# Kernel tuning notes

Measured on AMD Instinct MI355X. Metric: run time of the kernel, lower is better.

Reference implementation:

```python
import jax, jax.numpy as jnp
import numpy as np

B, H, W, C = 4, 64, 64, 256


def _conv1x1(t, w, b):
    # 1x1 Conv2D == per-pixel matmul over channels (NHWC)
    return jnp.einsum('bhwc,cd->bhwd', t, w) + b


def setup_inputs() -> dict:
    key = jax.random.key(0)
    ks = jax.random.split(key, 12)
    s = 0.02
    inp = {
        'x': jax.random.normal(ks[0], (B, H, W, C), dtype=jnp.float32),
        'g': jax.random.normal(ks[1], (B, H, W, C), dtype=jnp.float32),
        'Wx1': jax.random.normal(ks[2], (C, C), dtype=jnp.float32) * s,
        'bx1': jnp.zeros((C,), dtype=jnp.float32),
        'Wx2': jax.random.normal(ks[3], (C, C), dtype=jnp.float32) * s,
        'bx2': jnp.zeros((C,), dtype=jnp.float32),
        'Wx3': jax.random.normal(ks[4], (C, C), dtype=jnp.float32) * s,
        'bx3': jnp.zeros((C,), dtype=jnp.float32),
        'Wg1': jax.random.normal(ks[5], (C, C), dtype=jnp.float32) * s,
        'bg1': jnp.zeros((C,), dtype=jnp.float32),
        'Wg2': jax.random.normal(ks[6], (C, C), dtype=jnp.float32) * s,
        'bg2': jnp.zeros((C,), dtype=jnp.float32),
    }
    return inp


def reference(x, g, Wx1, bx1, Wx2, bx2, Wx3, bx3, Wg1, bg1, Wg2, bg2):
    b, h, w, c = x.shape
    hw = h * w
    # x-branch projections, flattened to (B, HW, C)
    xw1 = _conv1x1(x, Wx1, bx1).reshape(b, hw, c)
    xw2 = _conv1x1(x, Wx2, bx2).reshape(b, hw, c)
    xw3 = _conv1x1(x, Wx3, bx3).reshape(b, hw, c)
    # g-branch projections
    gw1 = _conv1x1(g, Wg1, bg1).reshape(b, hw, c)
    gw2 = _conv1x1(g, Wg2, bg2).reshape(b, hw, c)
    # Dot(axes=(2,1))([xw_2, xw_1^T]) -> (B, HW, HW), softmax over last axis
    x_attn = jax.nn.softmax(jnp.einsum('bic,bjc->bij', xw2, xw1), axis=-1)
    g_attn = jax.nn.softmax(jnp.einsum('bic,bjc->bij', gw2, gw1), axis=-1)
    # elementwise gate then renormalize
    attn = jax.nn.softmax(x_attn * g_attn, axis=-1)
    # Keras Dot(axes=1): contract axis 1 of attn with axis 1 of xw3
    # out[b, j, c] = sum_i attn[b, i, j] * xw3[b, i, c]
    out = jnp.einsum('bij,bic->bjc', attn, xw3).reshape(b, h, w, c)
    return x + out
```

## Files before the change

kernel.cpp:

```cpp
#include <hip/hip_runtime.h>

typedef float f32x4 __attribute__((ext_vector_type(4)));
typedef short s16x8 __attribute__((ext_vector_type(8)));
typedef unsigned int u32x4 __attribute__((ext_vector_type(4)));
typedef unsigned char u8;
typedef unsigned short u16;
typedef unsigned int u32;
typedef unsigned long long u64;

#define NPOS 4096
#define CCH  256
#define MTOT 16384
#define PBYTES ((size_t)NPOS * NPOS * 2)

#define SZ_F8   ((size_t)MTOT * 256)
#define O_F8    ((size_t)0)
#define O_WT    (O_F8   + 4 * SZ_F8)
#define O_XW3T  (O_WT   + (size_t)5*256*256*2)
#define O_ZX    (O_XW3T + (size_t)MTOT*256*2)
#define O_ZG    (O_ZX   + (size_t)8*MTOT*4)
#define O_ID    (O_ZG   + (size_t)8*MTOT*4)
#define O_Z2    (O_ID   + (size_t)MTOT*4)
#define O_IZ2   (O_Z2   + (size_t)64*MTOT*4)
#define O_P     (O_IZ2  + (size_t)MTOT*4)

__device__ __forceinline__ u16 f2bf(float f) {
    u32 u = __builtin_bit_cast(u32, f);
    u32 r = (u + 0x7FFFu + ((u >> 16) & 1u)) >> 16;
    return (u16)r;
}
__device__ __forceinline__ float bf2f(u16 h) {
    u32 u = ((u32)h) << 16;
    return __builtin_bit_cast(float, u);
}
__device__ __forceinline__ u32 pk2(float a, float b) {
    return (u32)f2bf(a) | ((u32)f2bf(b) << 16);
}
__device__ __forceinline__ f32x4 mfma_bf16(s16x8 a, s16x8 b, f32x4 c) {
    return __builtin_amdgcn_mfma_f32_16x16x32_bf16(a, b, c, 0, 0, 0);
}
__device__ __forceinline__ f32x4 mfma_fp8(long a, long b, f32x4 c) {
    return __builtin_amdgcn_mfma_f32_16x16x32_fp8_fp8(a, b, c, 0, 0, 0);
}
__device__ __forceinline__ int xcd_swz(int bid, int nwg) {
    return (bid & 7) * (nwg >> 3) + (bid >> 3);
}
__device__ __forceinline__ u32x4 ntld(const void* p) {
    return __builtin_nontemporal_load((const u32x4*)p);
}
__device__ __forceinline__ void ntst(void* p, u32x4 v) {
    __builtin_nontemporal_store(v, (u32x4*)p);
}

__global__ __launch_bounds__(256) void prep_w(
    const float* __restrict__ W0, const float* __restrict__ W1,
    const float* __restrict__ W2, const float* __restrict__ W3,
    const float* __restrict__ W4, u32* __restrict__ wT)
{
    const int p = blockIdx.x, kq = blockIdx.y, n = threadIdx.x;
    const float* W = (p==0)?W0:(p==1)?W1:(p==2)?W2:(p==3)?W3:W4;
#pragma unroll 4
    for (int kk = 0; kk < 32; ++kk) {
        int k = kq*64 + kk*2;
        float v0 = W[k*256 + n];
        float v1 = W[(k+1)*256 + n];
        wT[(p*65536 + n*256 + k) >> 1] = pk2(v0, v1);
    }
}

__global__ __launch_bounds__(256) void proj_kernel(
    const float* __restrict__ x, const float* __restrict__ g,
    const float* __restrict__ bb0, const float* __restrict__ bb1,
    const float* __restrict__ bb2, const float* __restrict__ bb3,
    const float* __restrict__ bb4,
    const u16* __restrict__ wT, u8* __restrict__ f8, u8* __restrict__ xw3T)
{
    const int branch = blockIdx.y;
    const int m0 = blockIdx.x * 128;
    const float* A = branch ? g : x;
    __shared__ u8 sA[128*512];
    __shared__ u8 sC[128*512];
    const int t = threadIdx.x;
    const int l = t & 63, lr = l & 15, lg = l >> 4;
    const int wv = t >> 6, wm = wv >> 1, wn = wv & 1;

    {
        const int m = t >> 1, h = t & 1;
        const float* src = &A[(size_t)(m0 + m) * 256 + h * 128];
        const u32 dbase = m * 512;
#pragma unroll
        for (int c = 0; c < 16; ++c) {
            float4 a = *(const float4*)(src + c*8);
            float4 b = *(const float4*)(src + c*8 + 4);
            u32 pk[4] = { pk2(a.x, a.y), pk2(a.z, a.w), pk2(b.x, b.y), pk2(b.z, b.w) };
            int kbyte = h*256 + c*16;
            *(uint4*)&sA[dbase + (kbyte ^ ((m & 7) << 4))] = *(uint4*)pk;
        }
    }
    __syncthreads();

    const int np = branch ? 2 : 3;
    for (int pp = 0; pp < np; ++pp) {
        const int p = branch ? 3 + pp : pp;
        const float* bias = (p==0)?bb0:(p==1)?bb1:(p==2)?bb2:(p==3)?bb3:bb4;
        f32x4 acc[4][8];
#pragma unroll
        for (int i = 0; i < 4; ++i)
#pragma unroll
            for (int j = 0; j < 8; ++j) acc[i][j] = (f32x4){0.f,0.f,0.f,0.f};

#pragma unroll
        for (int ks = 0; ks < 8; ++ks) {
            s16x8 af[4];
#pragma unroll
            for (int Mt = 0; Mt < 4; ++Mt) {
                int m = wm*64 + Mt*16 + lr;
                af[Mt] = *(const s16x8*)&sA[m*512 + ((ks*64 + lg*16) ^ ((m & 7) << 4))];
            }
#pragma unroll
            for (int Nt = 0; Nt < 8; ++Nt) {
                int n = wn*128 + Nt*16 + lr;
                s16x8 bf = *(const s16x8*)&wT[p*65536 + n*256 + ks*32 + lg*8];
#pragma unroll
                for (int Mt = 0; Mt < 4; ++Mt)
                    acc[Mt][Nt] = mfma_bf16(af[Mt], bf, acc[Mt][Nt]);
            }
        }
#pragma unroll
        for (int Nt = 0; Nt < 8; ++Nt) {
            float bv = bias[wn*128 + Nt*16 + lr];
#pragma unroll
            for (int Mt = 0; Mt < 4; ++Mt)
#pragma unroll
                for (int q = 0; q < 4; ++q) acc[Mt][Nt][q] += bv;
        }

        if (p == 2) {
#pragma unroll
            for (int Mt = 0; Mt < 4; ++Mt)
#pragma unroll
                for (int Nt = 0; Nt < 8; ++Nt) {
                    int n = wn*128 + Nt*16 + lr;
                    int mrow = m0 + wm*64 + Mt*16 + lg*4;
                    int bb = mrow >> 12, pos = mrow & 4095;
                    uint2 val;
                    val.x = pk2(acc[Mt][Nt][0], acc[Mt][Nt][1]);
                    val.y = pk2(acc[Mt][Nt][2], acc[Mt][Nt][3]);
                    *(uint2*)(xw3T + ((size_t)(bb*256 + n)*4096 + pos)*2) = val;
                }
        } else {
            const int fi = (p < 2) ? p : p - 1;
#pragma unroll
            for (int Mt = 0; Mt < 4; ++Mt)
#pragma unroll
                for (int Nt = 0; Nt < 8; ++Nt) {
                    int n = wn*128 + Nt*16 + lr;
#pragma unroll
                    for (int q = 0; q < 4; ++q) {
                        int m = wm*64 + Mt*16 + lg*4 + q;
                        *(u16*)&sC[m*512 + ((n*2) ^ ((m & 7) << 4))] = f2bf(acc[Mt][Nt][q]);
                    }
                }
            __syncthreads();
            {
                const int m = t >> 1, h = t & 1;
                u8* dst = f8 + (size_t)fi * SZ_F8 + (size_t)(m0 + m)*256 + h*128;
#pragma unroll
                for (int c = 0; c < 16; ++c) {
                    uint4 v = *(const uint4*)&sC[m*512 + ((h*256 + c*16) ^ ((m & 7) << 4))];
                    float fv[8] = { bf2f((u16)(v.x & 0xffff)), bf2f((u16)(v.x >> 16)),
                                    bf2f((u16)(v.y & 0xffff)), bf2f((u16)(v.y >> 16)),
                                    bf2f((u16)(v.z & 0xffff)), bf2f((u16)(v.z >> 16)),
                                    bf2f((u16)(v.w & 0xffff)), bf2f((u16)(v.w >> 16)) };
                    u32 o0 = 0, o1 = 0;
                    o0 = __builtin_amdgcn_cvt_pk_fp8_f32(fv[0], fv[1], o0, false);
                    o0 = __builtin_amdgcn_cvt_pk_fp8_f32(fv[2], fv[3], o0, true);
                    o1 = __builtin_amdgcn_cvt_pk_fp8_f32(fv[4], fv[5], o1, false);
                    o1 = __builtin_amdgcn_cvt_pk_fp8_f32(fv[6], fv[7], o1, true);
                    uint2 ov; ov.x = o0; ov.y = o1;
                    *(uint2*)(dst + c*8) = ov;
                }
            }
            __syncthreads();
        }
    }
}

__global__ __launch_bounds__(256, 3) void score_kernel(
    const u8* __restrict__ f8, float* __restrict__ ZxP, float* __restrict__ ZgP,
    u8* __restrict__ PT, int bbase, int big)
{
    const int sid = xcd_swz(blockIdx.x, gridDim.x);
    const int bz = sid >> 8, rem = sid & 255;
    const int batch = bbase + bz;
    const int iblk = rem & 31, js = rem >> 5;
    const int i0 = iblk * 128;
    const int t = threadIdx.x, l = t & 63, lr = l & 15, lg = l >> 4, w = t >> 6;
    const u8* Ax = f8 + SZ_F8*1 + ((size_t)(batch*NPOS + i0 + w*32))*256;
    const u8* Ag = f8 + SZ_F8*3 + ((size_t)(batch*NPOS + i0 + w*32))*256;
    const u8* Bx = f8 + SZ_F8*0 + ((size_t)(batch*NPOS))*256;
    const u8* Bg = f8 + SZ_F8*2 + ((size_t)(batch*NPOS))*256;
    u8* PTb = PT + (big ? (size_t)bz * PBYTES : 0);

    long ax[2][8], ag[2][8];
#pragma unroll
    for (int Mt = 0; Mt < 2; ++Mt)
#pragma unroll
        for (int ks = 0; ks < 8; ++ks) {
            ax[Mt][ks] = *(const long*)&Ax[(Mt*16 + lr)*256 + ks*32 + lg*8];
            ag[Mt][ks] = *(const long*)&Ag[(Mt*16 + lr)*256 + ks*32 + lg*8];
        }

    float zx[2][4], zg[2][4];
#pragma unroll
    for (int Mt = 0; Mt < 2; ++Mt)
#pragma unroll
        for (int q = 0; q < 4; ++q) { zx[Mt][q] = 0.f; zg[Mt][q] = 0.f; }

    __shared__ __attribute__((aligned(16))) u8 sb[16384];
    __shared__ __attribute__((aligned(16))) u8 pb[8192];
    for (int jc = 0; jc < 16; ++jc) {
        const int j0 = js*512 + jc*32;
#pragma unroll
        for (int rep = 0; rep < 4; ++rep) {
            int s = rep*256 + t;
            int br = s >> 9, s2 = s & 511;
            int jr = s2 >> 4, kb = (s2 & 15) << 4;
            const u8* src = (br ? Bg : Bx) + (size_t)(j0 + jr)*256 + kb;
            uint4 v = *(const uint4*)src;
            int a0 = br*8192 + jr*256 + (kb ^ ((jr & 15) << 3));
            *(u64*)&sb[a0]     = ((u64)v.y << 32) | v.x;
            *(u64*)&sb[a0 ^ 8] = ((u64)v.w << 32) | v.z;
        }
        __syncthreads();
        f32x4 cx[2][2], cg[2][2];
#pragma unroll
        for (int Mt = 0; Mt < 2; ++Mt)
#pragma unroll
            for (int jt = 0; jt < 2; ++jt) { cx[Mt][jt] = (f32x4){0,0,0,0}; cg[Mt][jt] = (f32x4){0,0,0,0}; }
#pragma unroll
        for (int ks = 0; ks < 8; ++ks)
#pragma unroll
            for (int jt = 0; jt < 2; ++jt) {
                int jrow = jt*16 + lr;
                int off = jrow*256 + ((ks*32 + lg*8) ^ ((jrow & 15) << 3));
                long bxv = *(const long*)&sb[off];
                long bgv = *(const long*)&sb[8192 + off];
#pragma unroll
                for (int Mt = 0; Mt < 2; ++Mt) {
                    cx[Mt][jt] = mfma_fp8(ax[Mt][ks], bxv, cx[Mt][jt]);
                    cg[Mt][jt] = mfma_fp8(ag[Mt][ks], bgv, cg[Mt][jt]);
                }
            }
#pragma unroll
        for (int Mt = 0; Mt < 2; ++Mt)
#pragma unroll
            for (int jt = 0; jt < 2; ++jt) {
                int jl = jt*16 + lr;
                float e[4];
#pragma unroll
                for (int q = 0; q < 4; ++q) {
                    float exv = __expf(cx[Mt][jt][q]);
                    float egv = __expf(cg[Mt][jt][q]);
                    zx[Mt][q] += exv;
                    zg[Mt][q] += egv;
                    e[q] = exv * egv;
                }
                u64 pk = (u64)pk2(e[0], e[1]) | ((u64)pk2(e[2], e[3]) << 32);
                int ioff = w*64 + Mt*32 + lg*8;
                *(u64*)&pb[jl*256 + (ioff ^ ((jl & 15) << 3))] = pk;
            }
        __syncthreads();
        {
            const int row = t >> 3, seg = t & 7;
            const int swz = (row & 15) << 3;
            u8* dst = PTb + (size_t)(j0 + row)*8192 + (size_t)i0*2 + seg*32;
#pragma unroll
            for (int h = 0; h < 2; ++h) {
                int a0 = row*256 + ((seg*32 + h*16) ^ swz);
                u64 lo = *(const u64*)&pb[a0];
                u64 hi = *(const u64*)&pb[a0 ^ 8];
                u32x4 o;
                o[0] = (u32)lo; o[1] = (u32)(lo >> 32);
                o[2] = (u32)hi; o[3] = (u32)(hi >> 32);
                ntst(dst + h*16, o);
            }
        }
        __syncthreads();
    }
#pragma unroll
    for (int Mt = 0; Mt < 2; ++Mt)
#pragma unroll
        for (int q = 0; q < 4; ++q)
#pragma unroll
            for (int o = 1; o < 16; o <<= 1) {
                zx[Mt][q] += __shfl_xor(zx[Mt][q], o, 64);
                zg[Mt][q] += __shfl_xor(zg[Mt][q], o, 64);
            }
    if (lr == 0) {
#pragma unroll
        for (int Mt = 0; Mt < 2; ++Mt)
#pragma unroll
            for (int q = 0; q < 4; ++q) {
                int gi = batch*NPOS + i0 + w*32 + Mt*16 + lg*4 + q;
                ZxP[js*MTOT + gi] = zx[Mt][q];
                ZgP[js*MTOT + gi] = zg[Mt][q];
            }
    }
}

__global__ __launch_bounds__(256) void merge_d(
    const float* __restrict__ ZxP, const float* __restrict__ ZgP,
    float* __restrict__ iD, int bbase)
{
    int gi = bbase*NPOS + blockIdx.x*256 + threadIdx.x;
    float zx = 0.f, zg = 0.f;
#pragma unroll
    for (int js = 0; js < 8; ++js) { zx += ZxP[js*MTOT + gi]; zg += ZgP[js*MTOT + gi]; }
    iD[gi] = 1.0f / (zx * zg);
}

__global__ __launch_bounds__(256) void zpass_kernel(
    u8* __restrict__ PT, const float* __restrict__ iD,
    float* __restrict__ z2P, int bbase, int big)
{
    const int sid = xcd_swz(blockIdx.x, gridDim.x);
    const int bz = sid >> 7, r = sid & 127;
    const int ih = r >> 6, js = r & 63;
    const int batch = bbase + bz;
    u8* base = PT + (big ? (size_t)bz * PBYTES : 0) + (size_t)(js*64)*8192;
    const int i = ih*2048 + threadIdx.x*8;
    f32x4 d0 = *(const f32x4*)&iD[batch*NPOS + i];
    f32x4 d1 = *(const f32x4*)&iD[batch*NPOS + i + 4];
    f32x4 z0 = (f32x4){0,0,0,0}, z1 = (f32x4){0,0,0,0};
#pragma unroll 4
    for (int jr = 0; jr < 64; ++jr) {
        u8* addr = base + (size_t)jr*8192 + (size_t)i*2;
        u32x4 v = ntld(addr);
        float p0 = __expf(bf2f((u16)(v[0] & 0xffff)) * d0[0]);
        float p1 = __expf(bf2f((u16)(v[0] >> 16))    * d0[1]);
        float p2 = __expf(bf2f((u16)(v[1] & 0xffff)) * d0[2]);
        float p3 = __expf(bf2f((u16)(v[1] >> 16))    * d0[3]);
        float p4 = __expf(bf2f((u16)(v[2] & 0xffff)) * d1[0]);
        float p5 = __expf(bf2f((u16)(v[2] >> 16))    * d1[1]);
        float p6 = __expf(bf2f((u16)(v[3] & 0xffff)) * d1[2]);
        float p7 = __expf(bf2f((u16)(v[3] >> 16))    * d1[3]);
        z0[0] += p0; z0[1] += p1; z0[2] += p2; z0[3] += p3;
        z1[0] += p4; z1[1] += p5; z1[2] += p6; z1[3] += p7;
        u32x4 o;
        o[0] = pk2(p0, p1); o[1] = pk2(p2, p3);
        o[2] = pk2(p4, p5); o[3] = pk2(p6, p7);
        ntst(addr, o);
    }
    float* dst = z2P + (size_t)js*MTOT + batch*NPOS + i;
    *(f32x4*)dst = z0;
    *(f32x4*)(dst + 4) = z1;
}

__global__ __launch_bounds__(256) void prep_iz2(
    const float* __restrict__ z2P, float* __restrict__ iZ2, int bbase)
{
    int gi = bbase*NPOS + blockIdx.x*256 + threadIdx.x;
    float s = 0.f;
#pragma unroll 8
    for (int js = 0; js < 64; ++js) s += z2P[js*MTOT + gi];
    iZ2[gi] = 1.0f / s;
}

__global__ __launch_bounds__(256) void scalev_ip(
    u8* __restrict__ xw3T, const float* __restrict__ iZ2, int bbase)
{
    int eg = blockIdx.x*256 + threadIdx.x;
    int bz = bbase + (eg >> 17);
    int rem = eg & 131071;
    int c = rem >> 9, i = (rem & 511) << 3;
    size_t off = ((size_t)(bz*256 + c)*4096 + i)*2;
    uint4 v = *(const uint4*)(xw3T + off);
    f32x4 z0 = *(const f32x4*)&iZ2[bz*NPOS + i];
    f32x4 z1 = *(const f32x4*)&iZ2[bz*NPOS + i + 4];
    uint4 r;
    r.x = pk2(bf2f((u16)(v.x & 0xffff))*z0[0], bf2f((u16)(v.x >> 16))*z0[1]);
    r.y = pk2(bf2f((u16)(v.y & 0xffff))*z0[2], bf2f((u16)(v.y >> 16))*z0[3]);
    r.z = pk2(bf2f((u16)(v.z & 0xffff))*z1[0], bf2f((u16)(v.z >> 16))*z1[1]);
    r.w = pk2(bf2f((u16)(v.w & 0xffff))*z1[2], bf2f((u16)(v.w >> 16))*z1[3]);
    *(uint4*)(xw3T + off) = r;
}

__global__ __launch_bounds__(256, 4) void pv_kernel(
    const u8* __restrict__ PT, const u8* __restrict__ xw3T,
    const float* __restrict__ x, float* __restrict__ out, int bbase, int big)
{
    const int sid = xcd_swz(blockIdx.x, gridDim.x);
    const int bz = sid >> 8, rem = sid & 255;
    const int batch = bbase + bz;
    const int j0 = (rem >> 2) * 64, c0 = (rem & 3) * 64;
    const u8* PTb = PT + (big ? (size_t)bz * PBYTES : 0);
    const u8* xw3Tb = xw3T + (size_t)batch * 256 * 4096 * 2;
    __shared__ __attribute__((aligned(16))) u8 sA[2][8192];
    __shared__ __attribute__((aligned(16))) u8 sB[2][8192];
    const int t = threadIdx.x, l = t & 63, lr = l & 15, lg = l >> 4;
    const int wv = t >> 6, wm = wv >> 1, wn = wv & 1;
    const int srow = t >> 3, sseg = t & 7;

    f32x4 acc[2][2];
#pragma unroll
    for (int Mt = 0; Mt < 2; ++Mt)
#pragma unroll
        for (int Nt = 0; Nt < 2; ++Nt) acc[Mt][Nt] = (f32x4){0,0,0,0};

    u32x4 ra[2], rb[2];
    {
#pragma unroll
        for (int rp = 0; rp < 2; ++rp) {
            int row = rp*32 + srow;
            ra[rp] = *(const u32x4*)(PTb + (size_t)(j0 + row)*8192 + (size_t)(sseg*8)*2);
            rb[rp] = *(const u32x4*)(xw3Tb + ((size_t)(c0 + row)*4096 + sseg*8)*2);
        }
    }
    for (int kt = 0; kt < 64; ++kt) {
        const int cur = kt & 1;
#pragma unroll
        for (int rp = 0; rp < 2; ++rp) {
            int row = rp*32 + srow;
            int ad = row*128 + ((sseg*16) ^ ((row & 7) << 4));
            *(u32x4*)&sA[cur][ad] = ra[rp];
            *(u32x4*)&sB[cur][ad] = rb[rp];
        }
        __syncthreads();
        if (kt < 63) {
            const int k0 = (kt + 1) * 64;
#pragma unroll
            for (int rp = 0; rp < 2; ++rp) {
                int row = rp*32 + srow;
                ra[rp] = *(const u32x4*)(PTb + (size_t)(j0 + row)*8192 + (size_t)(k0 + sseg*8)*2);
                rb[rp] = *(const u32x4*)(xw3Tb + ((size_t)(c0 + row)*4096 + k0 + sseg*8)*2);
            }
        }
#pragma unroll
        for (int ks = 0; ks < 2; ++ks) {
            s16x8 af[2], bf[2];
#pragma unroll
            for (int Mt = 0; Mt < 2; ++Mt) {
                int row = wm*32 + Mt*16 + lr;
                af[Mt] = *(const s16x8*)&sA[cur][row*128 + ((ks*64 + lg*16) ^ ((row & 7) << 4))];
            }
#pragma unroll
            for (int Nt = 0; Nt < 2; ++Nt) {
                int row = wn*32 + Nt*16 + lr;
                bf[Nt] = *(const s16x8*)&sB[cur][row*128 + ((ks*64 + lg*16) ^ ((row & 7) << 4))];
            }
#pragma unroll
            for (int Mt = 0; Mt < 2; ++Mt)
#pragma unroll
                for (int Nt = 0; Nt < 2; ++Nt)
                    acc[Mt][Nt] = mfma_bf16(af[Mt], bf[Nt], acc[Mt][Nt]);
        }
    }
#pragma unroll
    for (int Mt = 0; Mt < 2; ++Mt)
#pragma unroll
        for (int Nt = 0; Nt < 2; ++Nt)
#pragma unroll
            for (int q = 0; q < 4; ++q) {
                int j = j0 + wm*32 + Mt*16 + lg*4 + q;
                int c = c0 + wn*32 + Nt*16 + lr;
                size_t idx = ((size_t)(batch*NPOS + j))*256 + c;
                out[idx] = x[idx] + acc[Mt][Nt][q];
            }
}

extern "C" void kernel_launch(void* const* d_in, const int* in_sizes, int n_in,
                              void* d_out, int out_size, void* d_ws, size_t ws_size,
                              hipStream_t stream)
{
    const float* x = (const float*)d_in[0];
    const float* g = (const float*)d_in[1];
    const float* W[5]  = {(const float*)d_in[2], (const float*)d_in[4], (const float*)d_in[6],
                          (const float*)d_in[8], (const float*)d_in[10]};
    const float* Bi[5] = {(const float*)d_in[3], (const float*)d_in[5], (const float*)d_in[7],
                          (const float*)d_in[9], (const float*)d_in[11]};
    char* ws = (char*)d_ws;
    u8*  f8   = (u8*)(ws + O_F8);
    u16* wT   = (u16*)(ws + O_WT);
    u8*  xw3T = (u8*)(ws + O_XW3T);
    float* ZxP = (float*)(ws + O_ZX);
    float* ZgP = (float*)(ws + O_ZG);
    float* iD  = (float*)(ws + O_ID);
    float* z2P = (float*)(ws + O_Z2);
    float* iZ2 = (float*)(ws + O_IZ2);
    u8*  PT   = (u8*)(ws + O_P);
    float* out = (float*)d_out;

    const int big = (ws_size >= O_P + 4 * PBYTES) ? 1 : 0;

    prep_w<<<dim3(5,4), 256, 0, stream>>>(W[0], W[1], W[2], W[3], W[4], (u32*)wT);
    proj_kernel<<<dim3(128,2), 256, 0, stream>>>(x, g, Bi[0], Bi[1], Bi[2], Bi[3], Bi[4],
                                                 wT, f8, xw3T);
    if (big) {
        score_kernel<<<1024, 256, 0, stream>>>(f8, ZxP, ZgP, PT, 0, 1);
        merge_d<<<64, 256, 0, stream>>>(ZxP, ZgP, iD, 0);
        zpass_kernel<<<512, 256, 0, stream>>>(PT, iD, z2P, 0, 1);
        prep_iz2<<<64, 256, 0, stream>>>(z2P, iZ2, 0);
        scalev_ip<<<2048, 256, 0, stream>>>(xw3T, iZ2, 0);
        pv_kernel<<<1024, 256, 0, stream>>>(PT, xw3T, x, out, 0, 1);
    } else {
        for (int b = 0; b < 4; ++b) {
            score_kernel<<<256, 256, 0, stream>>>(f8, ZxP, ZgP, PT, b, 0);
            merge_d<<<16, 256, 0, stream>>>(ZxP, ZgP, iD, b);
            zpass_kernel<<<128, 256, 0, stream>>>(PT, iD, z2P, b, 0);
            prep_iz2<<<16, 256, 0, stream>>>(z2P, iZ2, b);
            scalev_ip<<<512, 256, 0, stream>>>(xw3T, iZ2, b);
            pv_kernel<<<256, 256, 0, stream>>>(PT, xw3T, x, out, b, 0);
        }
    }
}
```

Baseline: 290.5 us.

## Double-buffer B tiles and P staging to overlap loads, MFMA and stores

```diff
diff --git a/kernel.cpp b/kernel.cpp
--- a/kernel.cpp
+++ b/kernel.cpp
@@ -217,22 +217,68 @@
 #pragma unroll
         for (int q = 0; q < 4; ++q) { zx[Mt][q] = 0.f; zg[Mt][q] = 0.f; }
 
-    __shared__ __attribute__((aligned(16))) u8 sb[16384];
-    __shared__ __attribute__((aligned(16))) u8 pb[8192];
+    __shared__ __attribute__((aligned(16))) u8 sb[2][16384];
+    __shared__ __attribute__((aligned(16))) u8 pb[2][8192];
+
+    u32x4 st[4];
+    const int st_br = t >> 9;
+    (void)st_br;
+
+#define LOAD_REGS(JC)                                                         \
+    {                                                                         \
+        const int j0_ = js*512 + (JC)*32;                                     \
+        _Pragma("unroll")                                                     \
+        for (int rep = 0; rep < 4; ++rep) {                                   \
+            int s = rep*256 + t;                                              \
+            int br = s >> 9, s2 = s & 511;                                    \
+            int jr = s2 >> 4, kb = (s2 & 15) << 4;                            \
+            const u8* src = (br ? Bg : Bx) + (size_t)(j0_ + jr)*256 + kb;     \
+            st[rep] = *(const u32x4*)src;                                     \
+        }                                                                     \
+    }
+
+#define WRITE_SB(BUF)                                                         \
+    {                                                                         \
+        _Pragma("unroll")                                                     \
+        for (int rep = 0; rep < 4; ++rep) {                                   \
+            int s = rep*256 + t;                                              \
+            int br = s >> 9, s2 = s & 511;                                    \
+            int jr = s2 >> 4, kb = (s2 & 15) << 4;                            \
+            int a0 = br*8192 + jr*256 + (kb ^ ((jr & 15) << 3));              \
+            u64 lo = ((u64)st[rep][1] << 32) | st[rep][0];                    \
+            u64 hi = ((u64)st[rep][3] << 32) | st[rep][2];                    \
+            *(u64*)&sb[BUF][a0]     = lo;                                     \
+            *(u64*)&sb[BUF][a0 ^ 8] = hi;                                     \
+        }                                                                     \
+    }
+
+#define STORE_E(JC, BUF)                                                      \
+    {                                                                         \
+        const int j0_ = js*512 + (JC)*32;                                     \
+        const int row = t >> 3, seg = t & 7;                                  \
+        const int swz = (row & 15) << 3;                                      \
+        u8* dst = PTb + (size_t)(j0_ + row)*8192 + (size_t)i0*2 + seg*32;     \
+        _Pragma("unroll")                                                     \
+        for (int h = 0; h < 2; ++h) {                                         \
+            int a0 = row*256 + ((seg*32 + h*16) ^ swz);                       \
+            u64 lo = *(const u64*)&pb[BUF][a0];                               \
+            u64 hi = *(const u64*)&pb[BUF][a0 ^ 8];                           \
+            u32x4 o;                                                          \
+            o[0] = (u32)lo; o[1] = (u32)(lo >> 32);                           \
+            o[2] = (u32)hi; o[3] = (u32)(hi >> 32);                           \
+            ntst(dst + h*16, o);                                              \
+        }                                                                     \
+    }
+
+    LOAD_REGS(0);
+    WRITE_SB(0);
+
     for (int jc = 0; jc < 16; ++jc) {
-        const int j0 = js*512 + jc*32;
-#pragma unroll
-        for (int rep = 0; rep < 4; ++rep) {
-            int s = rep*256 + t;
-            int br = s >> 9, s2 = s & 511;
-            int jr = s2 >> 4, kb = (s2 & 15) << 4;
-            const u8* src = (br ? Bg : Bx) + (size_t)(j0 + jr)*256 + kb;
-            uint4 v = *(const uint4*)src;
-            int a0 = br*8192 + jr*256 + (kb ^ ((jr & 15) << 3));
-            *(u64*)&sb[a0]     = ((u64)v.y << 32) | v.x;
-            *(u64*)&sb[a0 ^ 8] = ((u64)v.w << 32) | v.z;
-        }
+        const int cur = jc & 1;
         __syncthreads();
+        if (jc < 15) LOAD_REGS(jc + 1);
+        if (jc > 0)  STORE_E(jc - 1, cur ^ 1);
+
         f32x4 cx[2][2], cg[2][2];
 #pragma unroll
         for (int Mt = 0; Mt < 2; ++Mt)
@@ -244,8 +290,8 @@
             for (int jt = 0; jt < 2; ++jt) {
                 int jrow = jt*16 + lr;
                 int off = jrow*256 + ((ks*32 + lg*8) ^ ((jrow & 15) << 3));
-                long bxv = *(const long*)&sb[off];
-                long bgv = *(const long*)&sb[8192 + off];
+                long bxv = *(const long*)&sb[cur][off];
+                long bgv = *(const long*)&sb[cur][8192 + off];
 #pragma unroll
                 for (int Mt = 0; Mt < 2; ++Mt) {
                     cx[Mt][jt] = mfma_fp8(ax[Mt][ks], bxv, cx[Mt][jt]);
@@ -268,26 +314,17 @@
                 }
                 u64 pk = (u64)pk2(e[0], e[1]) | ((u64)pk2(e[2], e[3]) << 32);
                 int ioff = w*64 + Mt*32 + lg*8;
-                *(u64*)&pb[jl*256 + (ioff ^ ((jl & 15) << 3))] = pk;
-            }
-        __syncthreads();
-        {
-            const int row = t >> 3, seg = t & 7;
-            const int swz = (row & 15) << 3;
-            u8* dst = PTb + (size_t)(j0 + row)*8192 + (size_t)i0*2 + seg*32;
-#pragma unroll
-            for (int h = 0; h < 2; ++h) {
-                int a0 = row*256 + ((seg*32 + h*16) ^ swz);
-                u64 lo = *(const u64*)&pb[a0];
-                u64 hi = *(const u64*)&pb[a0 ^ 8];
-                u32x4 o;
-                o[0] = (u32)lo; o[1] = (u32)(lo >> 32);
-                o[2] = (u32)hi; o[3] = (u32)(hi >> 32);
-                ntst(dst + h*16, o);
-            }
-        }
-        __syncthreads();
-    }
+                *(u64*)&pb[cur][jl*256 + (ioff ^ ((jl & 15) << 3))] = pk;
+            }
+        if (jc < 15) WRITE_SB(cur ^ 1);
+    }
+    __syncthreads();
+    STORE_E(15, 1);
+
+#undef LOAD_REGS
+#undef WRITE_SB
+#undef STORE_E
+
 #pragma unroll
     for (int Mt = 0; Mt < 2; ++Mt)
 #pragma unroll
```

Result: slower. 299.0 us (+2.9%).

## Recompute exp in PV load path instead of writing P back; fuse V scaling

Applied to the files above, without the earlier changes.

```diff
diff --git a/kernel.cpp b/kernel.cpp
--- a/kernel.cpp
+++ b/kernel.cpp
@@ -321,36 +321,29 @@
 }
 
 __global__ __launch_bounds__(256) void zpass_kernel(
-    u8* __restrict__ PT, const float* __restrict__ iD,
+    const u8* __restrict__ PT, const float* __restrict__ iD,
     float* __restrict__ z2P, int bbase, int big)
 {
     const int sid = xcd_swz(blockIdx.x, gridDim.x);
     const int bz = sid >> 7, r = sid & 127;
     const int ih = r >> 6, js = r & 63;
     const int batch = bbase + bz;
-    u8* base = PT + (big ? (size_t)bz * PBYTES : 0) + (size_t)(js*64)*8192;
+    const u8* base = PT + (big ? (size_t)bz * PBYTES : 0) + (size_t)(js*64)*8192;
     const int i = ih*2048 + threadIdx.x*8;
     f32x4 d0 = *(const f32x4*)&iD[batch*NPOS + i];
     f32x4 d1 = *(const f32x4*)&iD[batch*NPOS + i + 4];
     f32x4 z0 = (f32x4){0,0,0,0}, z1 = (f32x4){0,0,0,0};
 #pragma unroll 4
     for (int jr = 0; jr < 64; ++jr) {
-        u8* addr = base + (size_t)jr*8192 + (size_t)i*2;
-        u32x4 v = ntld(addr);
-        float p0 = __expf(bf2f((u16)(v[0] & 0xffff)) * d0[0]);
-        float p1 = __expf(bf2f((u16)(v[0] >> 16))    * d0[1]);
-        float p2 = __expf(bf2f((u16)(v[1] & 0xffff)) * d0[2]);
-        float p3 = __expf(bf2f((u16)(v[1] >> 16))    * d0[3]);
-        float p4 = __expf(bf2f((u16)(v[2] & 0xffff)) * d1[0]);
-        float p5 = __expf(bf2f((u16)(v[2] >> 16))    * d1[1]);
-        float p6 = __expf(bf2f((u16)(v[3] & 0xffff)) * d1[2]);
-        float p7 = __expf(bf2f((u16)(v[3] >> 16))    * d1[3]);
-        z0[0] += p0; z0[1] += p1; z0[2] += p2; z0[3] += p3;
-        z1[0] += p4; z1[1] += p5; z1[2] += p6; z1[3] += p7;
-        u32x4 o;
-        o[0] = pk2(p0, p1); o[1] = pk2(p2, p3);
-        o[2] = pk2(p4, p5); o[3] = pk2(p6, p7);
-        ntst(addr, o);
+        u32x4 v = ntld(base + (size_t)jr*8192 + (size_t)i*2);
+        z0[0] += __expf(bf2f((u16)(v[0] & 0xffff)) * d0[0]);
+        z0[1] += __expf(bf2f((u16)(v[0] >> 16))    * d0[1]);
+        z0[2] += __expf(bf2f((u16)(v[1] & 0xffff)) * d0[2]);
+        z0[3] += __expf(bf2f((u16)(v[1] >> 16))    * d0[3]);
+        z1[0] += __expf(bf2f((u16)(v[2] & 0xffff)) * d1[0]);
+        z1[1] += __expf(bf2f((u16)(v[2] >> 16))    * d1[1]);
+        z1[2] += __expf(bf2f((u16)(v[3] & 0xffff)) * d1[2]);
+        z1[3] += __expf(bf2f((u16)(v[3] >> 16))    * d1[3]);
     }
     float* dst = z2P + (size_t)js*MTOT + batch*NPOS + i;
     *(f32x4*)dst = z0;
@@ -367,27 +360,9 @@
     iZ2[gi] = 1.0f / s;
 }
 
-__global__ __launch_bounds__(256) void scalev_ip(
-    u8* __restrict__ xw3T, const float* __restrict__ iZ2, int bbase)
-{
-    int eg = blockIdx.x*256 + threadIdx.x;
-    int bz = bbase + (eg >> 17);
-    int rem = eg & 131071;
-    int c = rem >> 9, i = (rem & 511) << 3;
-    size_t off = ((size_t)(bz*256 + c)*4096 + i)*2;
-    uint4 v = *(const uint4*)(xw3T + off);
-    f32x4 z0 = *(const f32x4*)&iZ2[bz*NPOS + i];
-    f32x4 z1 = *(const f32x4*)&iZ2[bz*NPOS + i + 4];
-    uint4 r;
-    r.x = pk2(bf2f((u16)(v.x & 0xffff))*z0[0], bf2f((u16)(v.x >> 16))*z0[1]);
-    r.y = pk2(bf2f((u16)(v.y & 0xffff))*z0[2], bf2f((u16)(v.y >> 16))*z0[3]);
-    r.z = pk2(bf2f((u16)(v.z & 0xffff))*z1[0], bf2f((u16)(v.z >> 16))*z1[1]);
-    r.w = pk2(bf2f((u16)(v.w & 0xffff))*z1[2], bf2f((u16)(v.w >> 16))*z1[3]);
-    *(uint4*)(xw3T + off) = r;
-}
-
 __global__ __launch_bounds__(256, 4) void pv_kernel(
     const u8* __restrict__ PT, const u8* __restrict__ xw3T,
+    const float* __restrict__ iD, const float* __restrict__ iZ2,
     const float* __restrict__ x, float* __restrict__ out, int bbase, int big)
 {
     const int sid = xcd_swz(blockIdx.x, gridDim.x);
@@ -396,6 +371,8 @@
     const int j0 = (rem >> 2) * 64, c0 = (rem & 3) * 64;
     const u8* PTb = PT + (big ? (size_t)bz * PBYTES : 0);
     const u8* xw3Tb = xw3T + (size_t)batch * 256 * 4096 * 2;
+    const float* iDb = iD + batch*NPOS;
+    const float* iZb = iZ2 + batch*NPOS;
     __shared__ __attribute__((aligned(16))) u8 sA[2][8192];
     __shared__ __attribute__((aligned(16))) u8 sB[2][8192];
     const int t = threadIdx.x, l = t & 63, lr = l & 15, lg = l >> 4;
@@ -409,6 +386,7 @@
         for (int Nt = 0; Nt < 2; ++Nt) acc[Mt][Nt] = (f32x4){0,0,0,0};
 
     u32x4 ra[2], rb[2];
+    f32x4 rd0, rd1, rz0, rz1;
     {
 #pragma unroll
         for (int rp = 0; rp < 2; ++rp) {
@@ -416,6 +394,10 @@
             ra[rp] = *(const u32x4*)(PTb + (size_t)(j0 + row)*8192 + (size_t)(sseg*8)*2);
             rb[rp] = *(const u32x4*)(xw3Tb + ((size_t)(c0 + row)*4096 + sseg*8)*2);
         }
+        rd0 = *(const f32x4*)&iDb[sseg*8];
+        rd1 = *(const f32x4*)&iDb[sseg*8 + 4];
+        rz0 = *(const f32x4*)&iZb[sseg*8];
+        rz1 = *(const f32x4*)&iZb[sseg*8 + 4];
     }
     for (int kt = 0; kt < 64; ++kt) {
         const int cur = kt & 1;
@@ -423,18 +405,35 @@
         for (int rp = 0; rp < 2; ++rp) {
             int row = rp*32 + srow;
             int ad = row*128 + ((sseg*16) ^ ((row & 7) << 4));
-            *(u32x4*)&sA[cur][ad] = ra[rp];
-            *(u32x4*)&sB[cur][ad] = rb[rp];
+            u32x4 ea = ra[rp];
+            u32x4 oa;
+            oa[0] = pk2(__expf(bf2f((u16)(ea[0] & 0xffff))*rd0[0]), __expf(bf2f((u16)(ea[0] >> 16))*rd0[1]));
+            oa[1] = pk2(__expf(bf2f((u16)(ea[1] & 0xffff))*rd0[2]), __expf(bf2f((u16)(ea[1] >> 16))*rd0[3]));
+            oa[2] = pk2(__expf(bf2f((u16)(ea[2] & 0xffff))*rd1[0]), __expf(bf2f((u16)(ea[2] >> 16))*rd1[1]));
+            oa[3] = pk2(__expf(bf2f((u16)(ea[3] & 0xffff))*rd1[2]), __expf(bf2f((u16)(ea[3] >> 16))*rd1[3]));
+            *(u32x4*)&sA[cur][ad] = oa;
+            u32x4 eb = rb[rp];
+            u32x4 ob;
+            ob[0] = pk2(bf2f((u16)(eb[0] & 0xffff))*rz0[0], bf2f((u16)(eb[0] >> 16))*rz0[1]);
+            ob[1] = pk2(bf2f((u16)(eb[1] & 0xffff))*rz0[2], bf2f((u16)(eb[1] >> 16))*rz0[3]);
+            ob[2] = pk2(bf2f((u16)(eb[2] & 0xffff))*rz1[0], bf2f((u16)(eb[2] >> 16))*rz1[1]);
+            ob[3] = pk2(bf2f((u16)(eb[3] & 0xffff))*rz1[2], bf2f((u16)(eb[3] >> 16))*rz1[3]);
+            *(u32x4*)&sB[cur][ad] = ob;
         }
         __syncthreads();
         if (kt < 63) {
             const int k0 = (kt + 1) * 64;
+            const int ib = k0 + sseg*8;
 #pragma unroll
             for (int rp = 0; rp < 2; ++rp) {
                 int row = rp*32 + srow;
-                ra[rp] = *(const u32x4*)(PTb + (size_t)(j0 + row)*8192 + (size_t)(k0 + sseg*8)*2);
-                rb[rp] = *(const u32x4*)(xw3Tb + ((size_t)(c0 + row)*4096 + k0 + sseg*8)*2);
-            }
+                ra[rp] = *(const u32x4*)(PTb + (size_t)(j0 + row)*8192 + (size_t)ib*2);
+                rb[rp] = *(const u32x4*)(xw3Tb + ((size_t)(c0 + row)*4096 + ib)*2);
+            }
+            rd0 = *(const f32x4*)&iDb[ib];
+            rd1 = *(const f32x4*)&iDb[ib + 4];
+            rz0 = *(const f32x4*)&iZb[ib];
+            rz1 = *(const f32x4*)&iZb[ib + 4];
         }
 #pragma unroll
         for (int ks = 0; ks < 2; ++ks) {
@@ -501,16 +500,14 @@
         merge_d<<<64, 256, 0, stream>>>(ZxP, ZgP, iD, 0);
         zpass_kernel<<<512, 256, 0, stream>>>(PT, iD, z2P, 0, 1);
         prep_iz2<<<64, 256, 0, stream>>>(z2P, iZ2, 0);
-        scalev_ip<<<2048, 256, 0, stream>>>(xw3T, iZ2, 0);
-        pv_kernel<<<1024, 256, 0, stream>>>(PT, xw3T, x, out, 0, 1);
+        pv_kernel<<<1024, 256, 0, stream>>>(PT, xw3T, iD, iZ2, x, out, 0, 1);
     } else {
         for (int b = 0; b < 4; ++b) {
             score_kernel<<<256, 256, 0, stream>>>(f8, ZxP, ZgP, PT, b, 0);
             merge_d<<<16, 256, 0, stream>>>(ZxP, ZgP, iD, b);
             zpass_kernel<<<128, 256, 0, stream>>>(PT, iD, z2P, b, 0);
             prep_iz2<<<16, 256, 0, stream>>>(z2P, iZ2, b);
-            scalev_ip<<<512, 256, 0, stream>>>(xw3T, iZ2, b);
-            pv_kernel<<<256, 256, 0, stream>>>(PT, xw3T, x, out, b, 0);
-        }
-    }
-}
+            pv_kernel<<<256, 256, 0, stream>>>(PT, xw3T, iD, iZ2, x, out, b, 0);
+        }
+    }
+}
```

Result: slower. 315.2 us (+8.5%).
